# Optimization experiments

Measured on AMD Instinct MI355X. Metric: run time of the kernel, lower is better.

Reference implementation:

```python
import jax, jax.numpy as jnp
import numpy as np

N, F, B, D = 16384, 256, 48, 8


def setup_inputs() -> dict:
    key = jax.random.key(0)
    k_x, k_e, k_w, k_b = jax.random.split(key, 4)
    x = jax.random.normal(k_x, (N, F), dtype=jnp.float32)
    # per-feature sorted bin boundaries -> left edges and positive widths
    boundaries = jnp.sort(jax.random.uniform(k_e, (F, B + 1), dtype=jnp.float32,
                                             minval=-3.0, maxval=3.0), axis=-1)
    edges = boundaries[:, :-1]                     # [F, B]
    width = jnp.diff(boundaries, axis=-1)          # [F, B], > 0
    bound = 1.0 / np.sqrt(B)                       # nn.Linear default init
    W = jax.random.uniform(k_w, (F, B, D), dtype=jnp.float32, minval=-bound, maxval=bound)
    b = jax.random.uniform(k_b, (F, D), dtype=jnp.float32, minval=-bound, maxval=bound)
    return {"x": x, "edges": edges, "width": width, "W": W, "b": b}


def reference(x, edges, width, W, b):
    # piecewise-linear encoding: [N, F, B]
    h = (x[:, :, None] - edges) / width
    h = jnp.concatenate([
        jnp.minimum(h[..., :1], 1.0),          # first bin: clamp_max(1)
        jnp.clip(h[..., 1:-1], 0.0, 1.0),      # middle bins: clamp(0, 1)
        jnp.maximum(h[..., -1:], 0.0),         # last bin: clamp_min(0)
    ], axis=-1)
    # per-feature tiny Linear(B -> D), then concat over features
    out = jnp.einsum('nfb,fbd->nfd', h, W) + b   # [N, F, D]
    return out.reshape(x.shape[0], -1)           # [N, F*D]
```

## Files before the change

### kernel.cpp

```cpp
#include <hip/hip_runtime.h>


#define NN 16384
#define FF 256
#define BB 48
#define DD 8

#define FT 32
#define NT 1024
#define NSPLIT 64
#define NPB (NN / NSPLIT)
#define RPI 16
#define ITERS (NPB / RPI)

#define ESTR 52
#define RASTR 100
#define CSTR 396

__global__ __launch_bounds__(NT, 8)
void cple_kernel(const float* __restrict__ X,
                 const float* __restrict__ Edg,
                 const float* __restrict__ Wid,
                 const float* __restrict__ W,
                 const float* __restrict__ Bias,
                 float* __restrict__ Out)
{
    __shared__ float sE [FT * ESTR];
    __shared__ float sRA[FT * RASTR];
    __shared__ float sC [FT * CSTR];

    const int tid = threadIdx.x;
    const int f0  = blockIdx.x * FT;
    const int ns  = blockIdx.y;

    if (tid < FT * BB / 4) {
        const float4* E4 = (const float4*)(Edg + (size_t)f0 * BB);
        float4 v = E4[tid];
        int f = tid / 12, j4 = tid % 12;
        *(float4*)&sE[f * ESTR + j4 * 4] = v;
    }
    for (int idx = tid; idx < FT * BB; idx += NT) {
        int f = idx / BB, j = idx - f * BB;
        float e = Edg[(size_t)f0 * BB + idx];
        float w = Wid[(size_t)f0 * BB + idx];
        float r = 1.0f / w;
        sRA[f * RASTR + 2 * j]     = r;
        sRA[f * RASTR + 2 * j + 1] = -e * r;
    }
    {
        const float4* Wt4 = (const float4*)(W + (size_t)f0 * BB * DD);
        #pragma unroll
        for (int q = 0; q < 3; ++q) {
            int idx4 = tid + q * NT;
            float4 v = Wt4[idx4];
            int idx = idx4 * 4;
            int f   = idx / (BB * DD);
            int rem = idx - f * (BB * DD);
            *(float4*)&sC[f * CSTR + DD + rem] = v;
        }
    }

    const int h   = tid & 1;
    const int f_l = (tid >> 1) & 31;
    const int w_l = tid >> 6;

    const float* xp = X + (f0 + f_l);
    float* op = Out + (size_t)(f0 + f_l) * DD + h * 4;

    const int nbase = ns * NPB + w_l;
    float xn = xp[(size_t)nbase * FF];

    __syncthreads();

    const float* eF  = &sE [f_l * ESTR];
    const float* raF = &sRA[f_l * RASTR];
    const float* cF  = &sC [f_l * CSTR] + h * 4;
    float c4[11];
    #pragma unroll
    for (int m = 0; m < 11; ++m) c4[m] = eF[4 * (m + 1)];

    if (tid < FT * DD) {
        int f = tid >> 3, d = tid & 7;
        float* c = &sC[f * CSTR + d];
        float acc = Bias[(size_t)(f0 + f) * DD + d];
        c[0] = acc;
        #pragma unroll
        for (int ch = 0; ch < 3; ++ch) {
            float w[16];
            #pragma unroll
            for (int j = 0; j < 16; ++j) w[j] = c[(ch * 16 + j + 1) * DD];
            #pragma unroll
            for (int j = 0; j < 16; ++j) { acc += w[j]; c[(ch * 16 + j + 1) * DD] = acc; }
        }
    }
    __syncthreads();

    #pragma unroll
    for (int i = 0; i < ITERS; ++i) {
        int n = nbase + i * RPI;
        float xc = xn;
        if (i < ITERS - 1)
            xn = xp[(size_t)(n + RPI) * FF];

        int g = 0;
        #pragma unroll
        for (int m = 0; m < 11; ++m) g += (xc >= c4[m]) ? 1 : 0;
        int k4 = g * 4;

        float4 e = *(const float4*)(eF + k4);
        int k = k4 + (xc >= e.y) + (xc >= e.z) + (xc >= e.w);

        float2 ra = *(const float2*)(raF + 2 * k);
        const float* cK = cF + k * DD;
        float4 lo = *(const float4*)(cK);
        float4 hi = *(const float4*)(cK + DD);

        float t = fmaf(xc, ra.x, ra.y);

        float4 o;
        o.x = fmaf(t, hi.x - lo.x, lo.x);
        o.y = fmaf(t, hi.y - lo.y, lo.y);
        o.z = fmaf(t, hi.z - lo.z, lo.z);
        o.w = fmaf(t, hi.w - lo.w, lo.w);

        *(float4*)(op + (size_t)n * (FF * DD)) = o;
    }
}

extern "C" void kernel_launch(void* const* d_in, const int* in_sizes, int n_in,
                              void* d_out, int out_size, void* d_ws, size_t ws_size,
                              hipStream_t stream) {
    const float* x     = (const float*)d_in[0];
    const float* edges = (const float*)d_in[1];
    const float* width = (const float*)d_in[2];
    const float* W     = (const float*)d_in[3];
    const float* b     = (const float*)d_in[4];
    float* out = (float*)d_out;

    dim3 grid(FF / FT, NSPLIT);
    cple_kernel<<<grid, NT, 0, stream>>>(x, edges, width, W, b, out);
}
```

Before: 161.4 us.

## Split table precompute into separate kernel and read tables from global memory

Moves the per-feature cumulative weight table and reciprocal-width table construction into a small preceding kernel that writes them to workspace. The main kernel no longer stages edges, tables or weights in shared memory; each 512-thread block covers all 256 features for 16 rows and gathers its table entries directly from global memory, relying on the cache. This removes the redundant per-block table building and the barriers, but adds a second launch, a serial dependency on a tiny 4-block kernel, and uncoalesced per-lane global gathers in the hot loop.

```diff
diff --git a/kernel.cpp b/kernel.cpp
--- a/kernel.cpp
+++ b/kernel.cpp
@@ -6,109 +6,85 @@
 #define BB 48
 #define DD 8
 
-#define FT 32
-#define NT 1024
-#define NSPLIT 64
-#define NPB (NN / NSPLIT)
-#define RPI 16
-#define ITERS (NPB / RPI)
+#define CW_FLOATS (FF * (BB + 1) * DD)
+#define RA_FLOATS (FF * 2 * BB)
 
-#define ESTR 52
-#define RASTR 100
-#define CSTR 396
-
-__global__ __launch_bounds__(NT, 8)
-void cple_kernel(const float* __restrict__ X,
-                 const float* __restrict__ Edg,
+__global__ __launch_bounds__(512, 4)
+void cple_tables(const float* __restrict__ Edg,
                  const float* __restrict__ Wid,
                  const float* __restrict__ W,
                  const float* __restrict__ Bias,
-                 float* __restrict__ Out)
+                 float* __restrict__ ws)
 {
-    __shared__ float sE [FT * ESTR];
-    __shared__ float sRA[FT * RASTR];
-    __shared__ float sC [FT * CSTR];
+    const int tg = blockIdx.x * 512 + threadIdx.x;
+    const int f = tg >> 3, d = tg & 7;
+    float* CW = ws;
+    float* RA = ws + CW_FLOATS;
 
-    const int tid = threadIdx.x;
-    const int f0  = blockIdx.x * FT;
-    const int ns  = blockIdx.y;
+    float acc = Bias[(size_t)f * DD + d];
+    float* cf = CW + (size_t)f * ((BB + 1) * DD) + d;
+    cf[0] = acc;
+    const float* wf = W + (size_t)f * BB * DD + d;
+    #pragma unroll 8
+    for (int b = 0; b < BB; ++b) {
+        acc += wf[b * DD];
+        cf[(b + 1) * DD] = acc;
+    }
 
-    if (tid < FT * BB / 4) {
-        const float4* E4 = (const float4*)(Edg + (size_t)f0 * BB);
-        float4 v = E4[tid];
-        int f = tid / 12, j4 = tid % 12;
-        *(float4*)&sE[f * ESTR + j4 * 4] = v;
-    }
-    for (int idx = tid; idx < FT * BB; idx += NT) {
-        int f = idx / BB, j = idx - f * BB;
-        float e = Edg[(size_t)f0 * BB + idx];
-        float w = Wid[(size_t)f0 * BB + idx];
-        float r = 1.0f / w;
-        sRA[f * RASTR + 2 * j]     = r;
-        sRA[f * RASTR + 2 * j + 1] = -e * r;
-    }
-    {
-        const float4* Wt4 = (const float4*)(W + (size_t)f0 * BB * DD);
-        #pragma unroll
-        for (int q = 0; q < 3; ++q) {
-            int idx4 = tid + q * NT;
-            float4 v = Wt4[idx4];
-            int idx = idx4 * 4;
-            int f   = idx / (BB * DD);
-            int rem = idx - f * (BB * DD);
-            *(float4*)&sC[f * CSTR + DD + rem] = v;
+    if (d == 0) {
+        const float* ef = Edg + (size_t)f * BB;
+        const float* vf = Wid + (size_t)f * BB;
+        float2* raf = (float2*)(RA + (size_t)f * (2 * BB));
+        #pragma unroll 8
+        for (int j = 0; j < BB; ++j) {
+            float r = 1.0f / vf[j];
+            raf[j] = make_float2(r, -ef[j] * r);
         }
     }
+}
 
+#define ROWS_PB 16
+
+__global__ __launch_bounds__(512, 8)
+void cple_main(const float* __restrict__ X,
+               const float* __restrict__ Edg,
+               const float* __restrict__ ws,
+               float* __restrict__ Out)
+{
+    const int tid = threadIdx.x;
     const int h   = tid & 1;
-    const int f_l = (tid >> 1) & 31;
-    const int w_l = tid >> 6;
+    const int f   = tid >> 1;
+    const int row0 = blockIdx.x * ROWS_PB;
 
-    const float* xp = X + (f0 + f_l);
-    float* op = Out + (size_t)(f0 + f_l) * DD + h * 4;
+    const float* CW = ws;
+    const float* RA = ws + CW_FLOATS;
 
-    const int nbase = ns * NPB + w_l;
-    float xn = xp[(size_t)nbase * FF];
+    const float* eF  = Edg + (size_t)f * BB;
+    const float* raF = RA + (size_t)f * (2 * BB);
+    const float* cF  = CW + (size_t)f * ((BB + 1) * DD) + h * 4;
+    const float* xp  = X + f;
+    float* op = Out + (size_t)f * DD + h * 4;
 
-    __syncthreads();
-
-    const float* eF  = &sE [f_l * ESTR];
-    const float* raF = &sRA[f_l * RASTR];
-    const float* cF  = &sC [f_l * CSTR] + h * 4;
     float c4[11];
     #pragma unroll
     for (int m = 0; m < 11; ++m) c4[m] = eF[4 * (m + 1)];
 
-    if (tid < FT * DD) {
-        int f = tid >> 3, d = tid & 7;
-        float* c = &sC[f * CSTR + d];
-        float acc = Bias[(size_t)(f0 + f) * DD + d];
-        c[0] = acc;
-        #pragma unroll
-        for (int ch = 0; ch < 3; ++ch) {
-            float w[16];
-            #pragma unroll
-            for (int j = 0; j < 16; ++j) w[j] = c[(ch * 16 + j + 1) * DD];
-            #pragma unroll
-            for (int j = 0; j < 16; ++j) { acc += w[j]; c[(ch * 16 + j + 1) * DD] = acc; }
-        }
-    }
-    __syncthreads();
+    float xn = xp[(size_t)row0 * FF];
 
     #pragma unroll
-    for (int i = 0; i < ITERS; ++i) {
-        int n = nbase + i * RPI;
+    for (int i = 0; i < ROWS_PB; ++i) {
+        const int n = row0 + i;
         float xc = xn;
-        if (i < ITERS - 1)
-            xn = xp[(size_t)(n + RPI) * FF];
+        if (i < ROWS_PB - 1)
+            xn = xp[(size_t)(n + 1) * FF];
 
         int g = 0;
         #pragma unroll
         for (int m = 0; m < 11; ++m) g += (xc >= c4[m]) ? 1 : 0;
-        int k4 = g * 4;
+        const int k4 = g * 4;
 
         float4 e = *(const float4*)(eF + k4);
-        int k = k4 + (xc >= e.y) + (xc >= e.z) + (xc >= e.w);
+        const int k = k4 + (xc >= e.y) + (xc >= e.z) + (xc >= e.w);
 
         float2 ra = *(const float2*)(raF + 2 * k);
         const float* cK = cF + k * DD;
@@ -136,7 +112,8 @@
     const float* W     = (const float*)d_in[3];
     const float* b     = (const float*)d_in[4];
     float* out = (float*)d_out;
+    float* ws  = (float*)d_ws;
 
-    dim3 grid(FF / FT, NSPLIT);
-    cple_kernel<<<grid, NT, 0, stream>>>(x, edges, width, W, b, out);
+    cple_tables<<<dim3(4), dim3(512), 0, stream>>>(edges, width, W, b, ws);
+    cple_main<<<dim3(NN / ROWS_PB), dim3(512), 0, stream>>>(x, edges, ws, out);
 }
```

Measured after the change: 263.2 us. 63.0% more time.
